# Kernel tuning notes

Measured on AMD Instinct MI355X. Metric: run time of the kernel, lower is better.

## Reference

```python
import jax, jax.numpy as jnp
import numpy as np

N_NODES = 10000
N_REL = 50
R_AUG = 2 * N_REL + 1  # forward + inverse + self-loop relation
D_EMB = 128
D_H1 = 128
D_H2 = 128
N_EDGES = 320000
N_BATCH = 65536


def setup_inputs() -> dict:
    key = jax.random.key(0)
    ks = jax.random.split(key, 10)
    s = jax.random.randint(ks[0], (N_EDGES,), 0, N_NODES)
    p = jax.random.randint(ks[1], (N_EDGES,), 0, N_REL)
    o = jax.random.randint(ks[2], (N_EDGES,), 0, N_NODES)
    graph = jnp.stack([s, p, o], axis=1)  # [E,3] (subject, relation, object)
    bs = jax.random.randint(ks[3], (N_BATCH,), 0, N_NODES)
    bp = jax.random.randint(ks[4], (N_BATCH,), 0, N_REL)
    bo = jax.random.randint(ks[5], (N_BATCH,), 0, N_NODES)
    batch = jnp.stack([bs, bp, bo], axis=1)  # [B,3] triples to score
    node_embeddings = jax.random.normal(ks[6], (N_NODES, D_EMB), jnp.float32) * 0.02
    W1 = jax.random.normal(ks[7], (R_AUG, D_EMB, D_H1), jnp.float32) * 0.02
    b1 = jnp.zeros((D_H1,), jnp.float32)
    W2 = jax.random.normal(ks[8], (R_AUG, D_H1, D_H2), jnp.float32) * 0.02
    b2 = jnp.zeros((D_H2,), jnp.float32)
    relations = jax.random.normal(ks[9], (N_REL, D_H2), jnp.float32) * 0.02
    return {"graph": graph, "batch": batch, "node_embeddings": node_embeddings,
            "W1": W1, "b1": b1, "W2": W2, "b2": b2, "relations": relations}


def _augment_edges(graph):
    # Add inverse relations (r + N_REL) and self-loops (relation 2*N_REL),
    # matching torch-rgcn's num_relations = nrel*2 + 1 construction.
    s, p, o = graph[:, 0], graph[:, 1], graph[:, 2]
    loop = jnp.arange(N_NODES, dtype=graph.dtype)
    src = jnp.concatenate([s, o, loop])
    rel = jnp.concatenate([p, p + N_REL, jnp.full((N_NODES,), 2 * N_REL, graph.dtype)])
    dst = jnp.concatenate([o, s, loop])
    return src, rel, dst


def _rgcn_layer(x, src, rel, dst, W, b):
    # Per-(relation, target-node) row normalization 1/c_{i,r}, then
    # h_i = sum_r W_r^T * sum_{j in N_r(i)} x_j / c_{i,r} + b
    seg = rel * N_NODES + dst  # segment id over stacked (R*N) adjacency rows
    deg = jax.ops.segment_sum(jnp.ones_like(seg, dtype=x.dtype), seg,
                              num_segments=R_AUG * N_NODES)
    norm = 1.0 / jnp.maximum(deg, 1.0)
    msg = x[src] * norm[seg][:, None]                      # [Etot, d_in]
    agg = jax.ops.segment_sum(msg, seg, num_segments=R_AUG * N_NODES)
    agg = agg.reshape(R_AUG, N_NODES, -1)                  # [R, N, d_in]
    return jnp.einsum('rnd,rdo->no', agg, W) + b           # [N, d_out]


def reference(graph, batch, node_embeddings, W1, b1, W2, b2, relations):
    src, rel, dst = _augment_edges(graph)
    x = _rgcn_layer(node_embeddings, src, rel, dst, W1, b1)
    x = jax.nn.relu(x)
    x = _rgcn_layer(x, src, rel, dst, W2, b2)
    # DistMult scoring: gather s/p/o embeddings, elementwise multiply, reduce.
    s_e = x[batch[:, 0]]
    p_e = relations[batch[:, 1]]
    o_e = x[batch[:, 2]]
    return (s_e * p_e * o_e).sum(axis=1)  # [B]
```

## Files before the change

kernel.cpp:

```cpp
#include <hip/hip_runtime.h>

#define N_NODES 10000
#define N_RELS  50
#define R_AUG   101
#define D       128
#define N_EDGES 320000
#define E_AUG   650000
#define N_BATCH 65536

#define NBINS   N_NODES
#define NSB     ((NBINS + 255) / 256)
#define NP      (R_AUG * N_NODES)
#define NSB2    ((NP + 255) / 256)
#define GEMM_NBLK (101 + (E_AUG + 127) / 128)

#define PREPX_BLOCKS 5000
#define TW_BLOCKS    808
#define HIST_BLOCKS  2540

typedef short bf16x8 __attribute__((ext_vector_type(8)));
typedef float f32x4  __attribute__((ext_vector_type(4)));

__device__ __forceinline__ unsigned short f2bf(float f) {
    union { float f; unsigned int u; } v; v.f = f;
    unsigned int r = (v.u + 0x7FFFu + ((v.u >> 16) & 1u)) >> 16;
    return (unsigned short)r;
}
__device__ __forceinline__ float bf2f(unsigned short h) {
    union { unsigned int u; float f; } v; v.u = ((unsigned int)h) << 16;
    return v.f;
}
__device__ __forceinline__ float u2f(unsigned int u) {
    union { unsigned int u; float f; } v; v.u = u; return v.f;
}
__device__ __forceinline__ unsigned int f2u(float f) {
    union { float f; unsigned int u; } v; v.f = f; return v.u;
}

__device__ __forceinline__ void decode_edge(const int* __restrict__ g, int e,
                                            int& src, int& rel, int& dst) {
    if (e < N_EDGES)            { src = g[3*e];     rel = g[3*e+1];          dst = g[3*e+2]; }
    else if (e < 2*N_EDGES)     { int b = e - N_EDGES;
                                  src = g[3*b+2];   rel = g[3*b+1] + N_RELS; dst = g[3*b];   }
    else                        { int n = e - 2*N_EDGES; src = n; dst = n; rel = 2*N_RELS;   }
}


__global__ __launch_bounds__(256) void prep_all(const float* __restrict__ x,
                                                unsigned short* __restrict__ xb,
                                                float* __restrict__ h1, float* __restrict__ h2,
                                                const float* __restrict__ b1,
                                                const float* __restrict__ b2,
                                                const float* __restrict__ W1,
                                                const float* __restrict__ W2,
                                                unsigned short* __restrict__ W1t,
                                                unsigned short* __restrict__ W2t,
                                                const int* __restrict__ g,
                                                int* __restrict__ deg,
                                                int* __restrict__ flags) {
    __shared__ float tile[64][65];
    int b = blockIdx.x, t = threadIdx.x;
    if (b < PREPX_BLOCKS) {
        int i = b * 256 + t;
        xb[i] = f2bf(x[i]);
        int d = i & (D - 1);
        h1[i] = b1[d];
        h2[i] = b2[d];
    } else if (b < PREPX_BLOCKS + TW_BLOCKS) {
        int q = b - PREPX_BLOCKS;
        int d0 = (q & 1) * 64, o0 = ((q >> 1) & 1) * 64;
        int z = q >> 2;
        const float* W = (z < R_AUG) ? W1 : W2;
        unsigned short* Wt = (z < R_AUG) ? W1t : W2t;
        int r = (z < R_AUG) ? z : (z - R_AUG);
        int tx = t & 63, ty = t >> 6;
        #pragma unroll
        for (int i = ty; i < 64; i += 4)
            tile[i][tx] = W[((size_t)r * D + (d0 + i)) * D + (o0 + tx)];
        __syncthreads();
        #pragma unroll
        for (int i = ty; i < 64; i += 4)
            Wt[((size_t)r * D + (o0 + i)) * D + (d0 + tx)] = f2bf(tile[tx][i]);
    } else {
        int e = (b - PREPX_BLOCKS - TW_BLOCKS) * 256 + t;
        if (e < E_AUG) {
            int src, rel, dst;
            decode_edge(g, e, src, rel, dst);
            atomicAdd(&deg[rel * N_NODES + dst], 1);
            flags[rel * N_NODES + src] = 1;
        }
    }
}


__global__ __launch_bounds__(256) void scan_block(const int* __restrict__ deg,
                                                  int* __restrict__ offs,
                                                  int* __restrict__ partial) {
    __shared__ int wsum[4];
    int t = threadIdx.x, lane = t & 63, w = t >> 6;
    int i = blockIdx.x * 256 + t;
    int v = 0;
    if (i < NBINS) {
        for (int r = 0; r < R_AUG; r++) v += deg[r * N_NODES + i];
    }
    int incl = v;
    #pragma unroll
    for (int off = 1; off < 64; off <<= 1) {
        int u = __shfl_up(incl, off, 64);
        if (lane >= off) incl += u;
    }
    if (lane == 63) wsum[w] = incl;
    __syncthreads();
    int woff = 0;
    for (int k = 0; k < w; k++) woff += wsum[k];
    if (i < NBINS) offs[i] = woff + incl - v;
    if (t == 255) partial[blockIdx.x] = woff + incl;
}

__global__ __launch_bounds__(256) void scan_partial(int* __restrict__ partial) {
    __shared__ int wsum[4];
    int t = threadIdx.x, lane = t & 63, w = t >> 6;
    int v = (t < NSB) ? partial[t] : 0;
    int incl = v;
    #pragma unroll
    for (int off = 1; off < 64; off <<= 1) {
        int u = __shfl_up(incl, off, 64);
        if (lane >= off) incl += u;
    }
    if (lane == 63) wsum[w] = incl;
    __syncthreads();
    int woff = 0;
    for (int k = 0; k < w; k++) woff += wsum[k];
    if (t < NSB) partial[t] = woff + incl - v;
}

__global__ __launch_bounds__(256) void scan_add(int* __restrict__ offs,
                                                const int* __restrict__ partial,
                                                int* __restrict__ cursor) {
    int i = blockIdx.x * 256 + threadIdx.x;
    if (i < NBINS) {
        int v = offs[i] + partial[i >> 8];
        offs[i] = v;
        cursor[i] = v;
    }
    if (i == 0) offs[NBINS] = E_AUG;
}


__global__ __launch_bounds__(256) void pscan1(const int* __restrict__ flags,
                                              int* __restrict__ S,
                                              int* __restrict__ ppart) {
    __shared__ int wsum[4];
    int t = threadIdx.x, lane = t & 63, w = t >> 6;
    int i = blockIdx.x * 256 + t;
    int v = (i < NP) ? flags[i] : 0;
    int incl = v;
    #pragma unroll
    for (int off = 1; off < 64; off <<= 1) {
        int u = __shfl_up(incl, off, 64);
        if (lane >= off) incl += u;
    }
    if (lane == 63) wsum[w] = incl;
    __syncthreads();
    int woff = 0;
    for (int k = 0; k < w; k++) woff += wsum[k];
    if (i < NP) S[i] = woff + incl - v;
    if (t == 255) ppart[blockIdx.x] = woff + incl;
}

__global__ __launch_bounds__(256) void pscan2(int* __restrict__ ppart,
                                              int* __restrict__ S) {
    __shared__ int wsum[4];
    int t = threadIdx.x, lane = t & 63, w = t >> 6;
    int carry = 0;
    for (int base = 0; base < NSB2; base += 256) {
        int i = base + t;
        int v = (i < NSB2) ? ppart[i] : 0;
        int incl = v;
        #pragma unroll
        for (int off = 1; off < 64; off <<= 1) {
            int u = __shfl_up(incl, off, 64);
            if (lane >= off) incl += u;
        }
        if (lane == 63) wsum[w] = incl;
        __syncthreads();
        int woff = 0;
        for (int k = 0; k < w; k++) woff += wsum[k];
        if (i < NSB2) ppart[i] = carry + woff + incl - v;
        carry += wsum[0] + wsum[1] + wsum[2] + wsum[3];
        __syncthreads();
    }
    if (t == 0) S[NP] = carry;
}

__global__ __launch_bounds__(256) void pscan3(const int* __restrict__ flags,
                                              int* __restrict__ S,
                                              const int* __restrict__ ppart,
                                              int* __restrict__ pair_src) {
    int i = blockIdx.x * 256 + threadIdx.x;
    if (i >= NP) return;
    int s = S[i] + ppart[i >> 8];
    S[i] = s;
    if (flags[i]) pair_src[s] = i % N_NODES;
}

__global__ __launch_bounds__(256) void blk_kernel(const int* __restrict__ S,
                                                  int* __restrict__ rowbase,
                                                  int* __restrict__ rowcnt,
                                                  int* __restrict__ blkoffs) {
    __shared__ int wsum[4];
    int t = threadIdx.x, lane = t & 63, w = t >> 6;
    int nb = 0;
    if (t < R_AUG) {
        int base = S[t * N_NODES];
        int nxt  = S[(t + 1) * N_NODES];
        rowbase[t] = base;
        rowcnt[t]  = nxt - base;
        nb = (nxt - base + 127) >> 7;
    }
    int incl = nb;
    #pragma unroll
    for (int off = 1; off < 64; off <<= 1) {
        int u = __shfl_up(incl, off, 64);
        if (lane >= off) incl += u;
    }
    if (lane == 63) wsum[w] = incl;
    __syncthreads();
    int woff = 0;
    for (int k = 0; k < w; k++) woff += wsum[k];
    if (t < R_AUG) blkoffs[t] = woff + incl - nb;
    if (t == R_AUG) blkoffs[R_AUG] = woff + incl;
}

__global__ __launch_bounds__(256) void scatter_kernel(const int* __restrict__ g,
                                                      const int* __restrict__ deg,
                                                      const int* __restrict__ S,
                                                      int* __restrict__ cursor,
                                                      uint2* __restrict__ sorted) {
    int e = blockIdx.x * 256 + threadIdx.x;
    if (e >= E_AUG) return;
    int src, rel, dst;
    decode_edge(g, e, src, rel, dst);
    int pos = atomicAdd(&cursor[dst], 1);
    int dg = deg[rel * N_NODES + dst];
    uint2 rec;
    rec.x = (unsigned)S[rel * N_NODES + src];
    rec.y = f2u(1.0f / (float)dg);
    sorted[pos] = rec;
}

__global__ __launch_bounds__(256) void relu_conv(const float* __restrict__ h,
                                                 unsigned short* __restrict__ hb) {
    int i = blockIdx.x * 256 + threadIdx.x;
    hb[i] = f2bf(fmaxf(h[i], 0.0f));
}


__global__ __launch_bounds__(256, 4) void gemm_compact(const unsigned short* __restrict__ xb,
                                                       const unsigned short* __restrict__ Wt,
                                                       const int* __restrict__ pair_src,
                                                       const int* __restrict__ rowbase,
                                                       const int* __restrict__ rowcnt,
                                                       const int* __restrict__ blkoffs,
                                                       unsigned short* __restrict__ Zc) {
    int b = blockIdx.x;
    if (b >= blkoffs[R_AUG]) return;
    int lo = 0, hi = R_AUG;
    while (hi - lo > 1) {
        int mid = (lo + hi) >> 1;
        if (blkoffs[mid] <= b) lo = mid; else hi = mid;
    }
    int r = lo;
    int lb = b - blkoffs[r];
    int rbase = rowbase[r] + lb * 128;
    int nrows = rowcnt[r] - lb * 128; if (nrows > 128) nrows = 128;

    int t = threadIdx.x, wave = t >> 6, lane = t & 63;
    int lr = lane & 15, lq = lane >> 4;
    int no = (wave & 1) * 64;
    int tp = wave >> 1;
    const unsigned short* Wr = Wt + (size_t)r * D * D;

    int prow = ((lr >> 2) << 3) + (lr & 3);
    bf16x8 w0[4], w1[4], w2[4], w3[4];
    #pragma unroll
    for (int ks = 0; ks < 4; ks++) {
        size_t kb = ks * 32 + lq * 8;
        w0[ks] = *(const bf16x8*)(Wr + (size_t)(no + prow) * D + kb);
        w1[ks] = *(const bf16x8*)(Wr + (size_t)(no + prow + 4) * D + kb);
        w2[ks] = *(const bf16x8*)(Wr + (size_t)(no + 32 + prow) * D + kb);
        w3[ks] = *(const bf16x8*)(Wr + (size_t)(no + 32 + prow + 4) * D + kb);
    }

    for (int tile = tp; tile * 16 < nrows; tile += 2) {
        int row = tile * 16 + lr;
        int rc = (row < nrows) ? row : 0;
        int srcr = pair_src[rbase + rc];
        const unsigned short* xrow = xb + (size_t)srcr * D + lq * 8;
        bf16x8 a[4];
        #pragma unroll
        for (int ks = 0; ks < 4; ks++)
            a[ks] = *(const bf16x8*)(xrow + ks * 32);

        f32x4 c0 = {}, c1 = {}, c2 = {}, c3 = {};
        #pragma unroll
        for (int ks = 0; ks < 4; ks++) {
            c0 = __builtin_amdgcn_mfma_f32_16x16x32_bf16(w0[ks], a[ks], c0, 0, 0, 0);
            c1 = __builtin_amdgcn_mfma_f32_16x16x32_bf16(w1[ks], a[ks], c1, 0, 0, 0);
            c2 = __builtin_amdgcn_mfma_f32_16x16x32_bf16(w2[ks], a[ks], c2, 0, 0, 0);
            c3 = __builtin_amdgcn_mfma_f32_16x16x32_bf16(w3[ks], a[ks], c3, 0, 0, 0);
        }
        if (row < nrows) {
            unsigned short* zrow = Zc + ((size_t)(rbase + row) << 7);
            uint4 p0, p1;
            p0.x = (unsigned)f2bf(c0[0]) | ((unsigned)f2bf(c0[1]) << 16);
            p0.y = (unsigned)f2bf(c0[2]) | ((unsigned)f2bf(c0[3]) << 16);
            p0.z = (unsigned)f2bf(c1[0]) | ((unsigned)f2bf(c1[1]) << 16);
            p0.w = (unsigned)f2bf(c1[2]) | ((unsigned)f2bf(c1[3]) << 16);
            p1.x = (unsigned)f2bf(c2[0]) | ((unsigned)f2bf(c2[1]) << 16);
            p1.y = (unsigned)f2bf(c2[2]) | ((unsigned)f2bf(c2[3]) << 16);
            p1.z = (unsigned)f2bf(c3[0]) | ((unsigned)f2bf(c3[1]) << 16);
            p1.w = (unsigned)f2bf(c3[2]) | ((unsigned)f2bf(c3[3]) << 16);
            *(uint4*)(zrow + no + lq * 8) = p0;
            *(uint4*)(zrow + no + 32 + lq * 8) = p1;
        }
    }
}


__global__ __launch_bounds__(256) void agg_pass(const uint2* __restrict__ sorted,
                                                const int* __restrict__ offs,
                                                const unsigned short* __restrict__ Zc,
                                                float* __restrict__ h) {
    int w = threadIdx.x >> 6, lane = threadIdx.x & 63;
    int dst = blockIdx.x * 4 + w;
    if (dst >= N_NODES) return;
    int e0 = offs[dst], e1 = offs[dst + 1];
    if (e0 == e1) return;
    int g = lane >> 4, s = lane & 15;
    float acc[8] = {};

    for (int base = e0; base < e1; base += 64) {
        int n = e1 - base; if (n > 64) n = 64;
        uint2 rec = {0u, 0u};
        if (lane < n) rec = sorted[base + lane];
        int iters = (n + 3) >> 2;
        #pragma unroll 4
        for (int j = 0; j < iters; j++) {
            int ej = j * 4 + g;
            int ec = (ej < n) ? ej : (n - 1);
            unsigned zi = (unsigned)__shfl((int)rec.x, ec, 64);
            unsigned nb = (unsigned)__shfl((int)rec.y, ec, 64);
            float nrm = (ej < n) ? u2f(nb) : 0.0f;
            const unsigned short* zp = Zc + ((size_t)zi << 7) + s * 8;
            uint4 zv = *(const uint4*)zp;
            acc[0] += nrm * bf2f((unsigned short)(zv.x & 0xFFFFu));
            acc[1] += nrm * bf2f((unsigned short)(zv.x >> 16));
            acc[2] += nrm * bf2f((unsigned short)(zv.y & 0xFFFFu));
            acc[3] += nrm * bf2f((unsigned short)(zv.y >> 16));
            acc[4] += nrm * bf2f((unsigned short)(zv.z & 0xFFFFu));
            acc[5] += nrm * bf2f((unsigned short)(zv.z >> 16));
            acc[6] += nrm * bf2f((unsigned short)(zv.w & 0xFFFFu));
            acc[7] += nrm * bf2f((unsigned short)(zv.w >> 16));
        }
    }
    #pragma unroll
    for (int k = 0; k < 8; k++) {
        acc[k] += __shfl_down(acc[k], 16, 64);
        acc[k] += __shfl_down(acc[k], 32, 64);
    }
    if (g == 0) {
        float* hp = h + ((size_t)dst << 7) + s * 8;
        float4 h0 = *(float4*)hp, h1v = *(float4*)(hp + 4);
        h0.x += acc[0]; h0.y += acc[1]; h0.z += acc[2]; h0.w += acc[3];
        h1v.x += acc[4]; h1v.y += acc[5]; h1v.z += acc[6]; h1v.w += acc[7];
        *(float4*)hp = h0;
        *(float4*)(hp + 4) = h1v;
    }
}


__global__ __launch_bounds__(256) void score_kernel(const int* __restrict__ batch,
                                                    const float* __restrict__ h2,
                                                    const float* __restrict__ rels,
                                                    float* __restrict__ out) {
    int t = threadIdx.x;
    int wv = t >> 6, half = (t & 63) >> 5, sl = t & 31;
    int i = blockIdx.x * 8 + wv * 2 + half;
    int bs = batch[3*i], bp = batch[3*i+1], bo = batch[3*i+2];
    float4 s = *(const float4*)(h2   + (size_t)bs * D + sl * 4);
    float4 p = *(const float4*)(rels + (size_t)bp * D + sl * 4);
    float4 o = *(const float4*)(h2   + (size_t)bo * D + sl * 4);
    float v = s.x * p.x * o.x + s.y * p.y * o.y + s.z * p.z * o.z + s.w * p.w * o.w;
    #pragma unroll
    for (int off = 16; off > 0; off >>= 1) v += __shfl_down(v, off, 32);
    if (sl == 0) out[i] = v;
}


extern "C" void kernel_launch(void* const* d_in, const int* in_sizes, int n_in,
                              void* d_out, int out_size, void* d_ws, size_t ws_size,
                              hipStream_t stream) {
    const int*   graph = (const int*)  d_in[0];
    const int*   batch = (const int*)  d_in[1];
    const float* emb   = (const float*)d_in[2];
    const float* W1    = (const float*)d_in[3];
    const float* b1    = (const float*)d_in[4];
    const float* W2    = (const float*)d_in[5];
    const float* b2    = (const float*)d_in[6];
    const float* rels  = (const float*)d_in[7];
    float* out = (float*)d_out;

    char* base = (char*)d_ws;
    size_t off = 0;
    auto take = [&](size_t bytes) -> char* {
        char* q = base + off;
        off += (bytes + 255) & ~(size_t)255;
        return q;
    };
    int*            deg     = (int*)           take((size_t)NP * 4);
    int*            flags   = (int*)           take((size_t)NP * 4);
    int*            S       = (int*)           take((size_t)(NP + 1) * 4);
    int*            pair_src= (int*)           take((size_t)E_AUG * 4);
    int*            ppart   = (int*)           take((size_t)NSB2 * 4);
    int*            rowbase = (int*)           take((size_t)(R_AUG + 1) * 4);
    int*            rowcnt  = (int*)           take((size_t)(R_AUG + 1) * 4);
    int*            blkoffs = (int*)           take((size_t)(R_AUG + 2) * 4);
    unsigned short* xb      = (unsigned short*)take((size_t)N_NODES * D * 2);
    float*          h1      = (float*)         take((size_t)N_NODES * D * 4);
    float*          h2      = (float*)         take((size_t)N_NODES * D * 4);
    unsigned short* h1b     = (unsigned short*)take((size_t)N_NODES * D * 2);
    unsigned short* W1t     = (unsigned short*)take((size_t)R_AUG * D * D * 2);
    unsigned short* W2t     = (unsigned short*)take((size_t)R_AUG * D * D * 2);
    int*            offs    = (int*)           take((size_t)(NBINS + 1) * 4);
    int*            cursor  = (int*)           take((size_t)NBINS * 4);
    int*            part    = (int*)           take((size_t)NSB * 4);
    uint2*          sorted  = (uint2*)         take((size_t)E_AUG * 8);
    unsigned short* Zc      = (unsigned short*)take((size_t)E_AUG * D * 2);

    hipMemsetAsync(deg, 0, (size_t)NP * 4, stream);
    hipMemsetAsync(flags, 0, (size_t)NP * 4, stream);
    prep_all<<<dim3(PREPX_BLOCKS + TW_BLOCKS + HIST_BLOCKS), 256, 0, stream>>>(
        emb, xb, h1, h2, b1, b2, W1, W2, W1t, W2t, graph, deg, flags);
    scan_block<<<dim3(NSB), 256, 0, stream>>>(deg, offs, part);
    scan_partial<<<dim3(1), 256, 0, stream>>>(part);
    scan_add<<<dim3(NSB), 256, 0, stream>>>(offs, part, cursor);
    pscan1<<<dim3(NSB2), 256, 0, stream>>>(flags, S, ppart);
    pscan2<<<dim3(1), 256, 0, stream>>>(ppart, S);
    pscan3<<<dim3(NSB2), 256, 0, stream>>>(flags, S, ppart, pair_src);
    blk_kernel<<<dim3(1), 256, 0, stream>>>(S, rowbase, rowcnt, blkoffs);
    scatter_kernel<<<dim3((E_AUG + 255) / 256), 256, 0, stream>>>(graph, deg, S, cursor, sorted);

    gemm_compact<<<dim3(GEMM_NBLK), 256, 0, stream>>>(xb, W1t, pair_src, rowbase, rowcnt, blkoffs, Zc);
    agg_pass<<<dim3((N_NODES + 3) / 4), 256, 0, stream>>>(sorted, offs, Zc, h1);
    relu_conv<<<dim3((N_NODES * D) / 256), 256, 0, stream>>>(h1, h1b);
    gemm_compact<<<dim3(GEMM_NBLK), 256, 0, stream>>>(h1b, W2t, pair_src, rowbase, rowcnt, blkoffs, Zc);
    agg_pass<<<dim3((N_NODES + 3) / 4), 256, 0, stream>>>(sorted, offs, Zc, h2);
    score_kernel<<<dim3(N_BATCH / 8), 256, 0, stream>>>(batch, h2, rels, out);
}
```

Measured before the change: 395.3 us.

## Fuse scan kernels, fold bias and ReLU into aggregation, prefetch GEMM tiles

Merges the six prefix-scan launches into three combined kernels and merges the two memsets into one. Bias add and the ReLU+bf16 conversion move into agg_pass, which drops the h1/h2 bias initialization in prep_all, the fp32 h1 buffer and the relu_conv kernel. The GEMM block span doubles to 256 rows, with source indices preloaded and the next tile's activations prefetched. Occupancy hint drops to 3, so register pressure rises and the GEMM grid has fewer blocks.

```diff
diff --git a/kernel.cpp b/kernel.cpp
--- a/kernel.cpp
+++ b/kernel.cpp
@@ -12,7 +12,8 @@
 #define NSB     ((NBINS + 255) / 256)
 #define NP      (R_AUG * N_NODES)
 #define NSB2    ((NP + 255) / 256)
-#define GEMM_NBLK (101 + (E_AUG + 127) / 128)
+#define BSPAN   256
+#define GEMM_NBLK (101 + (E_AUG + BSPAN - 1) / BSPAN)
 
 #define PREPX_BLOCKS 5000
 #define TW_BLOCKS    808
@@ -48,9 +49,6 @@
 
 __global__ __launch_bounds__(256) void prep_all(const float* __restrict__ x,
                                                 unsigned short* __restrict__ xb,
-                                                float* __restrict__ h1, float* __restrict__ h2,
-                                                const float* __restrict__ b1,
-                                                const float* __restrict__ b2,
                                                 const float* __restrict__ W1,
                                                 const float* __restrict__ W2,
                                                 unsigned short* __restrict__ W1t,
@@ -63,9 +61,6 @@
     if (b < PREPX_BLOCKS) {
         int i = b * 256 + t;
         xb[i] = f2bf(x[i]);
-        int d = i & (D - 1);
-        h1[i] = b1[d];
-        h2[i] = b2[d];
     } else if (b < PREPX_BLOCKS + TW_BLOCKS) {
         int q = b - PREPX_BLOCKS;
         int d0 = (q & 1) * 64, o0 = ((q >> 1) & 1) * 64;
@@ -93,89 +88,21 @@
 }
 
 
-__global__ __launch_bounds__(256) void scan_block(const int* __restrict__ deg,
-                                                  int* __restrict__ offs,
-                                                  int* __restrict__ partial) {
-    __shared__ int wsum[4];
-    int t = threadIdx.x, lane = t & 63, w = t >> 6;
-    int i = blockIdx.x * 256 + t;
-    int v = 0;
-    if (i < NBINS) {
-        for (int r = 0; r < R_AUG; r++) v += deg[r * N_NODES + i];
-    }
-    int incl = v;
-    #pragma unroll
-    for (int off = 1; off < 64; off <<= 1) {
-        int u = __shfl_up(incl, off, 64);
-        if (lane >= off) incl += u;
-    }
-    if (lane == 63) wsum[w] = incl;
-    __syncthreads();
-    int woff = 0;
-    for (int k = 0; k < w; k++) woff += wsum[k];
-    if (i < NBINS) offs[i] = woff + incl - v;
-    if (t == 255) partial[blockIdx.x] = woff + incl;
-}
-
-__global__ __launch_bounds__(256) void scan_partial(int* __restrict__ partial) {
-    __shared__ int wsum[4];
-    int t = threadIdx.x, lane = t & 63, w = t >> 6;
-    int v = (t < NSB) ? partial[t] : 0;
-    int incl = v;
-    #pragma unroll
-    for (int off = 1; off < 64; off <<= 1) {
-        int u = __shfl_up(incl, off, 64);
-        if (lane >= off) incl += u;
-    }
-    if (lane == 63) wsum[w] = incl;
-    __syncthreads();
-    int woff = 0;
-    for (int k = 0; k < w; k++) woff += wsum[k];
-    if (t < NSB) partial[t] = woff + incl - v;
-}
-
-__global__ __launch_bounds__(256) void scan_add(int* __restrict__ offs,
-                                                const int* __restrict__ partial,
-                                                int* __restrict__ cursor) {
-    int i = blockIdx.x * 256 + threadIdx.x;
-    if (i < NBINS) {
-        int v = offs[i] + partial[i >> 8];
-        offs[i] = v;
-        cursor[i] = v;
-    }
-    if (i == 0) offs[NBINS] = E_AUG;
-}
-
-
-__global__ __launch_bounds__(256) void pscan1(const int* __restrict__ flags,
+__global__ __launch_bounds__(256) void scan_a(const int* __restrict__ deg,
+                                              int* __restrict__ offs,
+                                              int* __restrict__ part,
+                                              const int* __restrict__ flags,
                                               int* __restrict__ S,
                                               int* __restrict__ ppart) {
     __shared__ int wsum[4];
     int t = threadIdx.x, lane = t & 63, w = t >> 6;
-    int i = blockIdx.x * 256 + t;
-    int v = (i < NP) ? flags[i] : 0;
-    int incl = v;
-    #pragma unroll
-    for (int off = 1; off < 64; off <<= 1) {
-        int u = __shfl_up(incl, off, 64);
-        if (lane >= off) incl += u;
-    }
-    if (lane == 63) wsum[w] = incl;
-    __syncthreads();
-    int woff = 0;
-    for (int k = 0; k < w; k++) woff += wsum[k];
-    if (i < NP) S[i] = woff + incl - v;
-    if (t == 255) ppart[blockIdx.x] = woff + incl;
-}
-
-__global__ __launch_bounds__(256) void pscan2(int* __restrict__ ppart,
-                                              int* __restrict__ S) {
-    __shared__ int wsum[4];
-    int t = threadIdx.x, lane = t & 63, w = t >> 6;
-    int carry = 0;
-    for (int base = 0; base < NSB2; base += 256) {
-        int i = base + t;
-        int v = (i < NSB2) ? ppart[i] : 0;
+    int b = blockIdx.x;
+    if (b < NSB) {
+        int i = b * 256 + t;
+        int v = 0;
+        if (i < NBINS) {
+            for (int r = 0; r < R_AUG; r++) v += deg[r * N_NODES + i];
+        }
         int incl = v;
         #pragma unroll
         for (int off = 1; off < 64; off <<= 1) {
@@ -186,22 +113,93 @@
         __syncthreads();
         int woff = 0;
         for (int k = 0; k < w; k++) woff += wsum[k];
-        if (i < NSB2) ppart[i] = carry + woff + incl - v;
-        carry += wsum[0] + wsum[1] + wsum[2] + wsum[3];
+        if (i < NBINS) offs[i] = woff + incl - v;
+        if (t == 255) part[b] = woff + incl;
+    } else {
+        int pb = b - NSB;
+        int i = pb * 256 + t;
+        int v = (i < NP) ? flags[i] : 0;
+        int incl = v;
+        #pragma unroll
+        for (int off = 1; off < 64; off <<= 1) {
+            int u = __shfl_up(incl, off, 64);
+            if (lane >= off) incl += u;
+        }
+        if (lane == 63) wsum[w] = incl;
         __syncthreads();
-    }
-    if (t == 0) S[NP] = carry;
-}
-
-__global__ __launch_bounds__(256) void pscan3(const int* __restrict__ flags,
+        int woff = 0;
+        for (int k = 0; k < w; k++) woff += wsum[k];
+        if (i < NP) S[i] = woff + incl - v;
+        if (t == 255) ppart[pb] = woff + incl;
+    }
+}
+
+
+__global__ __launch_bounds__(256) void scan_b(int* __restrict__ part,
+                                              int* __restrict__ ppart,
+                                              int* __restrict__ S) {
+    __shared__ int wsum[4];
+    int t = threadIdx.x, lane = t & 63, w = t >> 6;
+    if (blockIdx.x == 0) {
+        int v = (t < NSB) ? part[t] : 0;
+        int incl = v;
+        #pragma unroll
+        for (int off = 1; off < 64; off <<= 1) {
+            int u = __shfl_up(incl, off, 64);
+            if (lane >= off) incl += u;
+        }
+        if (lane == 63) wsum[w] = incl;
+        __syncthreads();
+        int woff = 0;
+        for (int k = 0; k < w; k++) woff += wsum[k];
+        if (t < NSB) part[t] = woff + incl - v;
+    } else {
+        int carry = 0;
+        for (int base = 0; base < NSB2; base += 256) {
+            int i = base + t;
+            int v = (i < NSB2) ? ppart[i] : 0;
+            int incl = v;
+            #pragma unroll
+            for (int off = 1; off < 64; off <<= 1) {
+                int u = __shfl_up(incl, off, 64);
+                if (lane >= off) incl += u;
+            }
+            if (lane == 63) wsum[w] = incl;
+            __syncthreads();
+            int woff = 0;
+            for (int k = 0; k < w; k++) woff += wsum[k];
+            if (i < NSB2) ppart[i] = carry + woff + incl - v;
+            carry += wsum[0] + wsum[1] + wsum[2] + wsum[3];
+            __syncthreads();
+        }
+        if (t == 0) S[NP] = carry;
+    }
+}
+
+
+__global__ __launch_bounds__(256) void scan_c(int* __restrict__ offs,
+                                              const int* __restrict__ part,
+                                              int* __restrict__ cursor,
+                                              const int* __restrict__ flags,
                                               int* __restrict__ S,
                                               const int* __restrict__ ppart,
                                               int* __restrict__ pair_src) {
-    int i = blockIdx.x * 256 + threadIdx.x;
-    if (i >= NP) return;
-    int s = S[i] + ppart[i >> 8];
-    S[i] = s;
-    if (flags[i]) pair_src[s] = i % N_NODES;
+    int b = blockIdx.x, t = threadIdx.x;
+    if (b < NSB) {
+        int i = b * 256 + t;
+        if (i < NBINS) {
+            int v = offs[i] + part[i >> 8];
+            offs[i] = v;
+            cursor[i] = v;
+        }
+        if (i == 0) offs[NBINS] = E_AUG;
+    } else {
+        int i = (b - NSB) * 256 + t;
+        if (i >= NP) return;
+        int s = S[i] + ppart[(b - NSB)];
+        S[i] = s;
+        if (flags[i]) pair_src[s] = i % N_NODES;
+    }
 }
 
 __global__ __launch_bounds__(256) void blk_kernel(const int* __restrict__ S,
@@ -216,7 +214,7 @@
         int nxt  = S[(t + 1) * N_NODES];
         rowbase[t] = base;
         rowcnt[t]  = nxt - base;
-        nb = (nxt - base + 127) >> 7;
+        nb = (nxt - base + BSPAN - 1) / BSPAN;
     }
     int incl = nb;
     #pragma unroll
@@ -249,14 +247,8 @@
     sorted[pos] = rec;
 }
 
-__global__ __launch_bounds__(256) void relu_conv(const float* __restrict__ h,
-                                                 unsigned short* __restrict__ hb) {
-    int i = blockIdx.x * 256 + threadIdx.x;
-    hb[i] = f2bf(fmaxf(h[i], 0.0f));
-}
-
-
-__global__ __launch_bounds__(256, 4) void gemm_compact(const unsigned short* __restrict__ xb,
+
+__global__ __launch_bounds__(256, 3) void gemm_compact(const unsigned short* __restrict__ xb,
                                                        const unsigned short* __restrict__ Wt,
                                                        const int* __restrict__ pair_src,
                                                        const int* __restrict__ rowbase,
@@ -272,14 +264,21 @@
     }
     int r = lo;
     int lb = b - blkoffs[r];
-    int rbase = rowbase[r] + lb * 128;
-    int nrows = rowcnt[r] - lb * 128; if (nrows > 128) nrows = 128;
+    int rbase = rowbase[r] + lb * BSPAN;
+    int nrows = rowcnt[r] - lb * BSPAN; if (nrows > BSPAN) nrows = BSPAN;
 
     int t = threadIdx.x, wave = t >> 6, lane = t & 63;
     int lr = lane & 15, lq = lane >> 4;
     int no = (wave & 1) * 64;
     int tp = wave >> 1;
     const unsigned short* Wr = Wt + (size_t)r * D * D;
+
+    int srcs[8];
+    #pragma unroll
+    for (int i = 0; i < 8; i++) {
+        int row = (tp + 2 * i) * 16 + lr;
+        srcs[i] = pair_src[rbase + (row < nrows ? row : 0)];
+    }
 
     int prow = ((lr >> 2) << 3) + (lr & 3);
     bf16x8 w0[4], w1[4], w2[4], w3[4];
@@ -292,15 +291,25 @@
         w3[ks] = *(const bf16x8*)(Wr + (size_t)(no + 32 + prow + 4) * D + kb);
     }
 
-    for (int tile = tp; tile * 16 < nrows; tile += 2) {
-        int row = tile * 16 + lr;
-        int rc = (row < nrows) ? row : 0;
-        int srcr = pair_src[rbase + rc];
-        const unsigned short* xrow = xb + (size_t)srcr * D + lq * 8;
-        bf16x8 a[4];
-        #pragma unroll
-        for (int ks = 0; ks < 4; ks++)
-            a[ks] = *(const bf16x8*)(xrow + ks * 32);
+    bf16x8 a[4];
+    {
+        const unsigned short* x0 = xb + (size_t)srcs[0] * D + lq * 8;
+        #pragma unroll
+        for (int ks = 0; ks < 4; ks++) a[ks] = *(const bf16x8*)(x0 + ks * 32);
+    }
+
+    #pragma unroll
+    for (int i = 0; i < 8; i++) {
+        int tile = tp + 2 * i;
+        if (tile * 16 >= nrows) break;
+
+        bf16x8 an[4];
+        {
+            int ni = (i < 7) ? i + 1 : 7;
+            const unsigned short* xn = xb + (size_t)srcs[ni] * D + lq * 8;
+            #pragma unroll
+            for (int ks = 0; ks < 4; ks++) an[ks] = *(const bf16x8*)(xn + ks * 32);
+        }
 
         f32x4 c0 = {}, c1 = {}, c2 = {}, c3 = {};
         #pragma unroll
@@ -310,6 +319,7 @@
             c2 = __builtin_amdgcn_mfma_f32_16x16x32_bf16(w2[ks], a[ks], c2, 0, 0, 0);
             c3 = __builtin_amdgcn_mfma_f32_16x16x32_bf16(w3[ks], a[ks], c3, 0, 0, 0);
         }
+        int row = tile * 16 + lr;
         if (row < nrows) {
             unsigned short* zrow = Zc + ((size_t)(rbase + row) << 7);
             uint4 p0, p1;
@@ -324,6 +334,8 @@
             *(uint4*)(zrow + no + lq * 8) = p0;
             *(uint4*)(zrow + no + 32 + lq * 8) = p1;
         }
+        #pragma unroll
+        for (int ks = 0; ks < 4; ks++) a[ks] = an[ks];
     }
 }
 
@@ -331,12 +343,14 @@
 __global__ __launch_bounds__(256) void agg_pass(const uint2* __restrict__ sorted,
                                                 const int* __restrict__ offs,
                                                 const unsigned short* __restrict__ Zc,
-                                                float* __restrict__ h) {
+                                                const float* __restrict__ bias,
+                                                float* __restrict__ hf,
+                                                unsigned short* __restrict__ hb,
+                                                int dorelu) {
     int w = threadIdx.x >> 6, lane = threadIdx.x & 63;
     int dst = blockIdx.x * 4 + w;
     if (dst >= N_NODES) return;
     int e0 = offs[dst], e1 = offs[dst + 1];
-    if (e0 == e1) return;
     int g = lane >> 4, s = lane & 15;
     float acc[8] = {};
 
@@ -370,12 +384,24 @@
         acc[k] += __shfl_down(acc[k], 32, 64);
     }
     if (g == 0) {
-        float* hp = h + ((size_t)dst << 7) + s * 8;
-        float4 h0 = *(float4*)hp, h1v = *(float4*)(hp + 4);
-        h0.x += acc[0]; h0.y += acc[1]; h0.z += acc[2]; h0.w += acc[3];
-        h1v.x += acc[4]; h1v.y += acc[5]; h1v.z += acc[6]; h1v.w += acc[7];
-        *(float4*)hp = h0;
-        *(float4*)(hp + 4) = h1v;
+        float4 b0 = *(const float4*)(bias + s * 8);
+        float4 b1v = *(const float4*)(bias + s * 8 + 4);
+        float v0 = b0.x + acc[0], v1 = b0.y + acc[1], v2 = b0.z + acc[2], v3 = b0.w + acc[3];
+        float v4 = b1v.x + acc[4], v5 = b1v.y + acc[5], v6 = b1v.z + acc[6], v7 = b1v.w + acc[7];
+        if (dorelu) {
+            uint4 pk;
+            pk.x = (unsigned)f2bf(fmaxf(v0, 0.0f)) | ((unsigned)f2bf(fmaxf(v1, 0.0f)) << 16);
+            pk.y = (unsigned)f2bf(fmaxf(v2, 0.0f)) | ((unsigned)f2bf(fmaxf(v3, 0.0f)) << 16);
+            pk.z = (unsigned)f2bf(fmaxf(v4, 0.0f)) | ((unsigned)f2bf(fmaxf(v5, 0.0f)) << 16);
+            pk.w = (unsigned)f2bf(fmaxf(v6, 0.0f)) | ((unsigned)f2bf(fmaxf(v7, 0.0f)) << 16);
+            *(uint4*)(hb + ((size_t)dst << 7) + s * 8) = pk;
+        } else {
+            float* hp = hf + ((size_t)dst << 7) + s * 8;
+            float4 o0 = {v0, v1, v2, v3};
+            float4 o1 = {v4, v5, v6, v7};
+            *(float4*)hp = o0;
+            *(float4*)(hp + 4) = o1;
+        }
     }
 }
 
@@ -427,7 +453,6 @@
     int*            rowcnt  = (int*)           take((size_t)(R_AUG + 1) * 4);
     int*            blkoffs = (int*)           take((size_t)(R_AUG + 2) * 4);
     unsigned short* xb      = (unsigned short*)take((size_t)N_NODES * D * 2);
-    float*          h1      = (float*)         take((size_t)N_NODES * D * 4);
     float*          h2      = (float*)         take((size_t)N_NODES * D * 4);
     unsigned short* h1b     = (unsigned short*)take((size_t)N_NODES * D * 2);
     unsigned short* W1t     = (unsigned short*)take((size_t)R_AUG * D * D * 2);
@@ -438,23 +463,18 @@
     uint2*          sorted  = (uint2*)         take((size_t)E_AUG * 8);
     unsigned short* Zc      = (unsigned short*)take((size_t)E_AUG * D * 2);
 
-    hipMemsetAsync(deg, 0, (size_t)NP * 4, stream);
-    hipMemsetAsync(flags, 0, (size_t)NP * 4, stream);
+    hipMemsetAsync(deg, 0, (size_t)((char*)S - (char*)deg), stream);
     prep_all<<<dim3(PREPX_BLOCKS + TW_BLOCKS + HIST_BLOCKS), 256, 0, stream>>>(
-        emb, xb, h1, h2, b1, b2, W1, W2, W1t, W2t, graph, deg, flags);
-    scan_block<<<dim3(NSB), 256, 0, stream>>>(deg, offs, part);
-    scan_partial<<<dim3(1), 256, 0, stream>>>(part);
-    scan_add<<<dim3(NSB), 256, 0, stream>>>(offs, part, cursor);
-    pscan1<<<dim3(NSB2), 256, 0, stream>>>(flags, S, ppart);
-    pscan2<<<dim3(1), 256, 0, stream>>>(ppart, S);
-    pscan3<<<dim3(NSB2), 256, 0, stream>>>(flags, S, ppart, pair_src);
+        emb, xb, W1, W2, W1t, W2t, graph, deg, flags);
+    scan_a<<<dim3(NSB + NSB2), 256, 0, stream>>>(deg, offs, part, flags, S, ppart);
+    scan_b<<<dim3(2), 256, 0, stream>>>(part, ppart, S);
+    scan_c<<<dim3(NSB + NSB2), 256, 0, stream>>>(offs, part, cursor, flags, S, ppart, pair_src);
     blk_kernel<<<dim3(1), 256, 0, stream>>>(S, rowbase, rowcnt, blkoffs);
     scatter_kernel<<<dim3((E_AUG + 255) / 256), 256, 0, stream>>>(graph, deg, S, cursor, sorted);
 
     gemm_compact<<<dim3(GEMM_NBLK), 256, 0, stream>>>(xb, W1t, pair_src, rowbase, rowcnt, blkoffs, Zc);
-    agg_pass<<<dim3((N_NODES + 3) / 4), 256, 0, stream>>>(sorted, offs, Zc, h1);
-    relu_conv<<<dim3((N_NODES * D) / 256), 256, 0, stream>>>(h1, h1b);
+    agg_pass<<<dim3((N_NODES + 3) / 4), 256, 0, stream>>>(sorted, offs, Zc, b1, (float*)0, h1b, 1);
     gemm_compact<<<dim3(GEMM_NBLK), 256, 0, stream>>>(h1b, W2t, pair_src, rowbase, rowcnt, blkoffs, Zc);
-    agg_pass<<<dim3((N_NODES + 3) / 4), 256, 0, stream>>>(sorted, offs, Zc, h2);
+    agg_pass<<<dim3((N_NODES + 3) / 4), 256, 0, stream>>>(sorted, offs, Zc, b2, h2, (unsigned short*)0, 0);
     score_kernel<<<dim3(N_BATCH / 8), 256, 0, stream>>>(batch, h2, rels, out);
 }
```

Result: faster. 360.0 us (-8.9%).
